# Optimization experiments

Hardware: AMD Instinct MI355X
Metric: run time of the kernel (lower is better)

Reference implementation:

```python
import jax, jax.numpy as jnp
import numpy as np

N_NODES = 100000
N_EDGES = 1600000
N_GRAPHS = 256
EPS = 1e-5  # GraphNorm / BatchNorm eps


def _seg_sum(x, seg, n):
    return jax.ops.segment_sum(x, seg, num_segments=n)


def setup_inputs() -> dict:
    key = jax.random.key(0)
    ks = jax.random.split(key, 24)
    f32 = jnp.float32

    def nrm(k, shape, s=0.05):
        return jax.random.normal(k, shape, f32) * s

    inp = {}
    inp["x"] = jax.random.normal(ks[0], (N_NODES, 64), f32)
    inp["edge_attr"] = jax.random.normal(ks[1], (N_EDGES, 8), f32)
    # edge_mlp: Linear(8,16) -> ReLU -> Linear(16,1); final bias +2 keeps degrees positive
    inp["em_w1"] = nrm(ks[2], (16, 8), 0.1); inp["em_b1"] = jnp.zeros((16,), f32)
    inp["em_w2"] = nrm(ks[3], (1, 16), 0.1); inp["em_b2"] = jnp.full((1,), 2.0, f32)
    # GCNConv weights stored (in, out); PyG GCNConv lin has no bias, separate bias after aggregation
    inp["conv_w0"] = nrm(ks[4], (64, 128)); inp["conv_b0"] = jnp.zeros((128,), f32)
    inp["conv_w1"] = nrm(ks[5], (128, 128)); inp["conv_b1"] = jnp.zeros((128,), f32)
    inp["conv_w2"] = nrm(ks[6], (128, 128)); inp["conv_b2"] = jnp.zeros((128,), f32)
    # GraphNorm params: weight=1, bias=0, mean_scale=1 (PyG init)
    for i in range(3):
        inp[f"gn_w{i}"] = jnp.ones((128,), f32)
        inp[f"gn_b{i}"] = jnp.zeros((128,), f32)
        inp[f"gn_ms{i}"] = jnp.ones((128,), f32)
    # MLP head (weights stored (in,out)); BatchNorm1d eval: running_mean=0, running_var=1
    inp["lin_w0"] = nrm(ks[7], (128, 256)); inp["lin_b0"] = jnp.zeros((256,), f32)
    inp["bn_g0"] = jnp.ones((256,), f32); inp["bn_b0"] = jnp.zeros((256,), f32)
    inp["lin_w1"] = nrm(ks[8], (256, 128)); inp["lin_b1"] = jnp.zeros((128,), f32)
    inp["bn_g1"] = jnp.ones((128,), f32); inp["bn_b1"] = jnp.zeros((128,), f32)
    inp["out_w"] = nrm(ks[9], (128, 1)); inp["out_b"] = jnp.zeros((1,), f32)
    inp["edge_index"] = jax.random.randint(ks[10], (2, N_EDGES), 0, N_NODES)
    inp["batch"] = jnp.sort(jax.random.randint(ks[11], (N_NODES,), 0, N_GRAPHS))
    return inp


def _gcn_conv(h, W, b, src, tgt, ew):
    # PyG GCNConv with edge_weight: add self-loops (weight 1), symmetric normalization
    hw = h @ W  # [N, out]
    deg = _seg_sum(ew, tgt, N_NODES) + 1.0  # in-degree incl. self-loop
    dinv = jnp.where(deg > 0, jax.lax.rsqrt(deg), 0.0)
    norm_e = dinv[src] * ew * dinv[tgt]  # [E]
    agg = _seg_sum(norm_e[:, None] * hw[src], tgt, N_NODES)
    agg = agg + (dinv * dinv)[:, None] * hw  # self-loop contribution
    return agg + b


def _graph_norm(h, batch, w, b, ms, cnt):
    mean = _seg_sum(h, batch, N_GRAPHS) / cnt[:, None]  # [G, C]
    sub = h - ms * mean[batch]
    var = _seg_sum(sub * sub, batch, N_GRAPHS) / cnt[:, None]
    return w * sub / jnp.sqrt(var + EPS)[batch] + b


def reference(x, edge_attr, em_w1, em_b1, em_w2, em_b2,
              conv_w0, conv_b0, conv_w1, conv_b1, conv_w2, conv_b2,
              gn_w0, gn_b0, gn_ms0, gn_w1, gn_b1, gn_ms1, gn_w2, gn_b2, gn_ms2,
              lin_w0, lin_b0, bn_g0, bn_b0, lin_w1, lin_b1, bn_g1, bn_b1,
              out_w, out_b, edge_index, batch):
    src, tgt = edge_index[0], edge_index[1]
    ew = (jax.nn.relu(edge_attr @ em_w1.T + em_b1) @ em_w2.T + em_b2).reshape(-1)  # [E]
    cnt = jnp.maximum(_seg_sum(jnp.ones((N_NODES,), x.dtype), batch, N_GRAPHS), 1.0)

    h = x
    layers = [(conv_w0, conv_b0, gn_w0, gn_b0, gn_ms0),
              (conv_w1, conv_b1, gn_w1, gn_b1, gn_ms1),
              (conv_w2, conv_b2, gn_w2, gn_b2, gn_ms2)]
    for W, b, gw, gb, gms in layers:
        h = _gcn_conv(h, W, b, src, tgt, ew)
        h = _graph_norm(h, batch, gw, gb, gms, cnt)
        h = jax.nn.relu(h)  # dropout is identity in eval mode

    pooled = _seg_sum(h, batch, N_GRAPHS) / cnt[:, None]  # global_mean_pool [G, 128]

    inv = 1.0 / jnp.sqrt(1.0 + EPS)  # BatchNorm1d eval: mean=0, var=1
    h = jax.nn.relu((pooled @ lin_w0 + lin_b0) * inv * bn_g0 + bn_b0)
    h = jax.nn.relu((h @ lin_w1 + lin_b1) * inv * bn_g1 + bn_b1)
    out = h @ out_w + out_b  # [G, 1]
    return (out, h)
```

## Files before the change

### kernel.cpp

```cpp
#include <hip/hip_runtime.h>

#define N_NODES 100000
#define N_EDGES 1600000
#define N_GRAPHS 256
#define EPS 1e-5f

#define NBUCK 1024
#define NUSED 782
#define NBLK 256
#define EPB (N_EDGES / NBLK)

#define WB 128
#define W0B 32
#define SB 2
#define PREP_BLOCKS (WB + W0B + SB + NBLK)

typedef __attribute__((ext_vector_type(8))) short bfrag8;
typedef __attribute__((ext_vector_type(4))) float facc4;

__device__ __forceinline__ void fma4(float4& a, float s, const float4& w) {
  a.x += s * w.x; a.y += s * w.y; a.z += s * w.z; a.w += s * w.w;
}

__device__ __forceinline__ unsigned short f2bf(float f) {
  union { float f; unsigned u; } x;
  x.f = f;
  unsigned r = x.u + 0x7FFF + ((x.u >> 16) & 1);
  return (unsigned short)(r >> 16);
}
__device__ __forceinline__ unsigned packbf(float a, float b) {
  return (unsigned)f2bf(a) | ((unsigned)f2bf(b) << 16);
}
__device__ __forceinline__ float4 bf4(unsigned lo, unsigned hi) {
  union { unsigned u; float f; } a, b, c, d;
  a.u = lo << 16;
  b.u = lo & 0xFFFF0000u;
  c.u = hi << 16;
  d.u = hi & 0xFFFF0000u;
  return make_float4(a.f, b.f, c.f, d.f);
}
__device__ __forceinline__ float bfat(const unsigned* tb, int idx) {
  unsigned u = tb[idx >> 1];
  union { unsigned u; float f; } v;
  v.u = (idx & 1) ? (u & 0xFFFF0000u) : (u << 16);
  return v.f;
}

__global__ __launch_bounds__(256) void k_prep(
    const float* __restrict__ cw1, const float* __restrict__ cw2,
    unsigned short* __restrict__ wt1, unsigned short* __restrict__ wt2,
    const float* __restrict__ cw0, unsigned short* __restrict__ wt0,
    const int* __restrict__ batch, int* __restrict__ start,
    const int* __restrict__ tgt, int* __restrict__ hists) {
  __shared__ int h[NBUCK];
  const int b = blockIdx.x;
  const int t = threadIdx.x;
  if (b < WB) {
    int half = b >> 6;
    int id = (b & 63) * 256 + t;
    const float* w = half ? cw2 : cw1;
    unsigned short* o = half ? wt2 : wt1;
    int n = id >> 7, k = id & 127;
    o[n * 128 + k] = f2bf(w[k * 128 + n]);
  } else if (b < WB + W0B) {
    int id = (b - WB) * 256 + t;
    if (id >= 8192) return;
    int n = id >> 6, k = id & 63;
    wt0[n * 64 + k] = f2bf(cw0[k * 128 + n]);
  } else if (b < WB + W0B + SB) {
    int g = (b - WB - W0B) * 256 + t;
    if (g > N_GRAPHS) return;
    int lo = 0, hi = N_NODES;
    while (lo < hi) {
      int mid = (lo + hi) >> 1;
      if (batch[mid] < g) lo = mid + 1; else hi = mid;
    }
    start[g] = lo;
  } else {
    const int blk = b - WB - W0B - SB;
    for (int i = t; i < NBUCK; i += 256) h[i] = 0;
    __syncthreads();
    const int s = blk * EPB, e = s + EPB;
    for (int j = s + t; j < e; j += 256) atomicAdd(&h[tgt[j] >> 7], 1);
    __syncthreads();
    for (int i = t; i < NBUCK; i += 256) hists[blk * NBUCK + i] = h[i];
  }
}

__global__ __launch_bounds__(1024) void k_bscan(const int* __restrict__ hists,
                                                int* __restrict__ bbase,
                                                int* __restrict__ cursor) {
  __shared__ int s[NBUCK];
  const int b = threadIdx.x;
  int tot = 0;
  for (int k = 0; k < NBLK; ++k) tot += hists[k * NBUCK + b];
  s[b] = tot;
  __syncthreads();
  for (int off = 1; off < NBUCK; off <<= 1) {
    int u = (b >= off) ? s[b - off] : 0;
    __syncthreads();
    s[b] += u;
    __syncthreads();
  }
  int base = s[b] - tot;
  bbase[b] = base;
  if (b == NBUCK - 1) bbase[NBUCK] = N_EDGES;
  int c = base;
  for (int k = 0; k < NBLK; ++k) {
    cursor[k * NBUCK + b] = c;
    c += hists[k * NBUCK + b];
  }
}

__global__ __launch_bounds__(256) void k_scatter(
    const float* __restrict__ ea, const float* __restrict__ w1,
    const float* __restrict__ b1, const float* __restrict__ w2,
    const float* __restrict__ b2, const int* __restrict__ src,
    const int* __restrict__ tgt, const int* __restrict__ cursor,
    uint2* __restrict__ mb) {
  __shared__ float W1[128], B1[16], W2[16];
  __shared__ int cur[NBUCK];
  const int blk = blockIdx.x, t = threadIdx.x;
  if (t < 128) W1[t] = w1[t];
  if (t < 16) { B1[t] = b1[t]; W2[t] = w2[t]; }
  for (int i = t; i < NBUCK; i += 256) cur[i] = cursor[blk * NBUCK + i];
  __syncthreads();
  const int s = blk * EPB, e = s + EPB;
  for (int j = s + t; j < e; j += 256) {
    const float4* ap = (const float4*)(ea + (size_t)j * 8);
    float4 a0 = ap[0], a1 = ap[1];
    float a[8] = {a0.x, a0.y, a0.z, a0.w, a1.x, a1.y, a1.z, a1.w};
    float out = b2[0];
#pragma unroll
    for (int i = 0; i < 16; ++i) {
      float h = B1[i];
#pragma unroll
      for (int jj = 0; jj < 8; ++jj) h += a[jj] * W1[i * 8 + jj];
      out += fmaxf(h, 0.f) * W2[i];
    }
    int d = tgt[j];
    int bin = d >> 7;
    int pos = atomicAdd(&cur[bin], 1);
    union { float f; unsigned u; } w;
    w.f = out;
    mb[pos] = make_uint2(w.u, (unsigned)src[j] | ((unsigned)(d & 127) << 25));
  }
}

__global__ __launch_bounds__(256) void k_csr(const uint2* __restrict__ mb,
                                             const int* __restrict__ bbase,
                                             uint2* __restrict__ meta,
                                             int* __restrict__ rowstart,
                                             float* __restrict__ dinv) {
  __shared__ int hist[128];
  __shared__ float degf[128];
  __shared__ int cur[128];
  const int b = blockIdx.x;
  const int t = threadIdx.x;
  const int s = bbase[b], e = bbase[b + 1];
  if (t < 128) { hist[t] = 0; degf[t] = 0.f; }
  __syncthreads();
  for (int j = s + t; j < e; j += 256) {
    uint2 m = mb[j];
    int bin = m.y >> 25;
    atomicAdd(&hist[bin], 1);
    union { unsigned u; float f; } w;
    w.u = m.x;
    atomicAdd(&degf[bin], w.f);
  }
  __syncthreads();
  int own = (t < 128) ? hist[t] : 0;
  for (int off = 1; off < 128; off <<= 1) {
    int u = (t >= off && t < 128) ? hist[t - off] : 0;
    __syncthreads();
    if (t < 128) hist[t] += u;
    __syncthreads();
  }
  if (t < 128) {
    int excl = hist[t] - own;
    int node = b * 128 + t;
    if (node <= N_NODES) rowstart[node] = s + excl;
    if (node < N_NODES) {
      float d = 1.f + degf[t];
      dinv[node] = d > 0.f ? rsqrtf(d) : 0.f;
    }
    cur[t] = s + excl;
  }
  __syncthreads();
  for (int j = s + t; j < e; j += 256) {
    uint2 m = mb[j];
    int bin = m.y >> 25;
    int pos = atomicAdd(&cur[bin], 1);
    meta[pos] = make_uint2(m.x, m.y & 0x1FFFFFFu);
  }
}

__global__ __launch_bounds__(256) void k_cvt(const float* __restrict__ x,
                                             const float* __restrict__ dinv,
                                             unsigned* __restrict__ xb) {
  int i = blockIdx.x * 256 + threadIdx.x;
  if (i >= N_NODES * 8) return;
  int n = i >> 3;
  float dv = dinv[n];
  const float4* p = (const float4*)(x + (size_t)i * 8);
  float4 a = p[0], b = p[1];
  uint4 o;
  o.x = packbf(dv * a.x, dv * a.y);
  o.y = packbf(dv * a.z, dv * a.w);
  o.z = packbf(dv * b.x, dv * b.y);
  o.w = packbf(dv * b.z, dv * b.w);
  ((uint4*)xb)[i] = o;
}

__global__ __launch_bounds__(256) void k_gather64b(
    const unsigned* __restrict__ xb, const uint2* __restrict__ meta,
    const int* __restrict__ rowstart, const float* __restrict__ dinv,
    unsigned* __restrict__ aggxb) {
  const int t = threadIdx.x;
  const int n = blockIdx.x * 4 + (t >> 6);
  if (n >= N_NODES) return;
  const unsigned lane = t & 63;
  const unsigned q = lane >> 3;
  const unsigned cl = lane & 7;
  const int rs = rowstart[n], re = rowstart[n + 1];
  const uint4* x4 = (const uint4*)xb;
  float4 lo0 = make_float4(0.f, 0.f, 0.f, 0.f), hi0 = lo0;
  float4 lo1 = lo0, hi1 = lo0;
  int j = rs;
  for (; j + 16 <= re; j += 16) {
    uint2 m0 = meta[j + q], m1 = meta[j + 8 + q];
    union { unsigned u; float f; } w0, w1;
    w0.u = m0.x; w1.u = m1.x;
    uint4 v0 = x4[(m0.y << 3) + cl];
    uint4 v1 = x4[(m1.y << 3) + cl];
    fma4(lo0, w0.f, bf4(v0.x, v0.y));
    fma4(hi0, w0.f, bf4(v0.z, v0.w));
    fma4(lo1, w1.f, bf4(v1.x, v1.y));
    fma4(hi1, w1.f, bf4(v1.z, v1.w));
  }
  for (; j + 8 <= re; j += 8) {
    uint2 m0 = meta[j + q];
    union { unsigned u; float f; } w0;
    w0.u = m0.x;
    uint4 v0 = x4[(m0.y << 3) + cl];
    fma4(lo0, w0.f, bf4(v0.x, v0.y));
    fma4(hi0, w0.f, bf4(v0.z, v0.w));
  }
  if (j + (int)q < re) {
    uint2 m0 = meta[j + q];
    union { unsigned u; float f; } w0;
    w0.u = m0.x;
    uint4 v0 = x4[(m0.y << 3) + cl];
    fma4(lo1, w0.f, bf4(v0.x, v0.y));
    fma4(hi1, w0.f, bf4(v0.z, v0.w));
  }
  lo0.x += lo1.x; lo0.y += lo1.y; lo0.z += lo1.z; lo0.w += lo1.w;
  hi0.x += hi1.x; hi0.y += hi1.y; hi0.z += hi1.z; hi0.w += hi1.w;
#pragma unroll
  for (int m = 8; m <= 32; m <<= 1) {
    lo0.x += __shfl_xor(lo0.x, m);
    lo0.y += __shfl_xor(lo0.y, m);
    lo0.z += __shfl_xor(lo0.z, m);
    lo0.w += __shfl_xor(lo0.w, m);
    hi0.x += __shfl_xor(hi0.x, m);
    hi0.y += __shfl_xor(hi0.y, m);
    hi0.z += __shfl_xor(hi0.z, m);
    hi0.w += __shfl_xor(hi0.w, m);
  }
  if (q == 0) {
    float dv = dinv[n];
    uint4 sv = x4[((unsigned)n << 3) + cl];
    float4 slo = bf4(sv.x, sv.y), shi = bf4(sv.z, sv.w);
    uint4 o;
    o.x = packbf(dv * (lo0.x + slo.x), dv * (lo0.y + slo.y));
    o.y = packbf(dv * (lo0.z + slo.z), dv * (lo0.w + slo.w));
    o.z = packbf(dv * (hi0.x + shi.x), dv * (hi0.y + shi.y));
    o.w = packbf(dv * (hi0.z + shi.z), dv * (hi0.w + shi.w));
    ((uint4*)aggxb)[((unsigned)n << 3) + cl] = o;
  }
}

__global__ __launch_bounds__(256) void k_hw_mfma0(
    const unsigned short* __restrict__ aggxb,
    const unsigned short* __restrict__ wt0, const float* __restrict__ bias,
    unsigned short* __restrict__ h1b) {
  __shared__ unsigned short Asb[64][72];
  __shared__ unsigned short Wsb[128][72];
  const int t = threadIdx.x;
  const int base = blockIdx.x * 64;

  for (int i = t; i < 1024; i += 256) {
    int nr = i >> 3, k8 = (i & 7) * 8;
    *(uint4*)&Wsb[nr][k8] = *(const uint4*)&wt0[nr * 64 + k8];
  }
  {
    const int ln = t >> 2;
    const int kp = (t & 3) * 16;
    const int n = base + ln;
    if (n < N_NODES) {
      *(uint4*)&Asb[ln][kp] = *(const uint4*)&aggxb[(size_t)n * 64 + kp];
      *(uint4*)&Asb[ln][kp + 8] = *(const uint4*)&aggxb[(size_t)n * 64 + kp + 8];
    } else {
      uint4 z = make_uint4(0, 0, 0, 0);
      *(uint4*)&Asb[ln][kp] = z;
      *(uint4*)&Asb[ln][kp + 8] = z;
    }
  }
  __syncthreads();

  const int wv = t >> 6;
  const int lr = t & 15;
  const int lk = (t >> 4) & 3;
  const int m0 = wv * 16;

  bfrag8 af[2];
#pragma unroll
  for (int kc = 0; kc < 2; ++kc)
    af[kc] = *(const bfrag8*)&Asb[m0 + lr][kc * 32 + lk * 8];

#pragma unroll
  for (int nt = 0; nt < 8; ++nt) {
    facc4 c = {0.f, 0.f, 0.f, 0.f};
#pragma unroll
    for (int kc = 0; kc < 2; ++kc) {
      bfrag8 bf = *(const bfrag8*)&Wsb[nt * 16 + lr][kc * 32 + lk * 8];
      c = __builtin_amdgcn_mfma_f32_16x16x32_bf16(af[kc], bf, c, 0, 0, 0);
    }
    int col = nt * 16 + lr;
    float bv = bias[col];
#pragma unroll
    for (int r = 0; r < 4; ++r) {
      int n = base + m0 + lk * 4 + r;
      if (n < N_NODES) h1b[(size_t)n * 128 + col] = f2bf(c[r] + bv);
    }
  }
}

__global__ __launch_bounds__(256) void k_hw_mfma(
    const unsigned* __restrict__ hb, const unsigned short* __restrict__ wt,
    const int* __restrict__ batch, const float* __restrict__ An,
    const float* __restrict__ Bn, const float* __restrict__ dinv,
    unsigned short* __restrict__ hwb) {
  __shared__ unsigned short Asb[64][136];
  __shared__ unsigned short Wsb[128][136];
  const int t = threadIdx.x;
  const int base = blockIdx.x * 64;

  for (int i = t; i < 2048; i += 256) {
    int nr = i >> 4, k8 = (i & 15) * 8;
    *(uint4*)&Wsb[nr][k8] = *(const uint4*)&wt[nr * 128 + k8];
  }
  {
    const int ln = t >> 2;
    const int cg = (t & 3) * 32;
    const int n = base + ln;
    if (n < N_NODES) {
      const int g = batch[n];
      const uint4* hp = (const uint4*)(hb + (size_t)n * 64);
      const float* Ap = An + (size_t)g * 128;
      const float* Bp = Bn + (size_t)g * 128;
#pragma unroll
      for (int qq = 0; qq < 4; ++qq) {
        int c = cg + qq * 8;
        uint4 v = hp[(t & 3) * 4 + qq];
        float4 lo = bf4(v.x, v.y);
        float4 hi = bf4(v.z, v.w);
        float4 Alo = *(const float4*)&Ap[c], Blo = *(const float4*)&Bp[c];
        float4 Ahi = *(const float4*)&Ap[c + 4], Bhi = *(const float4*)&Bp[c + 4];
        uint4 o;
        o.x = packbf(fmaxf(Alo.x * lo.x + Blo.x, 0.f),
                     fmaxf(Alo.y * lo.y + Blo.y, 0.f));
        o.y = packbf(fmaxf(Alo.z * lo.z + Blo.z, 0.f),
                     fmaxf(Alo.w * lo.w + Blo.w, 0.f));
        o.z = packbf(fmaxf(Ahi.x * hi.x + Bhi.x, 0.f),
                     fmaxf(Ahi.y * hi.y + Bhi.y, 0.f));
        o.w = packbf(fmaxf(Ahi.z * hi.z + Bhi.z, 0.f),
                     fmaxf(Ahi.w * hi.w + Bhi.w, 0.f));
        *(uint4*)&Asb[ln][c] = o;
      }
    } else {
      uint4 z = make_uint4(0, 0, 0, 0);
#pragma unroll
      for (int qq = 0; qq < 4; ++qq) *(uint4*)&Asb[ln][cg + qq * 8] = z;
    }
  }
  __syncthreads();

  const int wv = t >> 6;
  const int lr = t & 15;
  const int lk = (t >> 4) & 3;
  const int m0 = wv * 16;

  bfrag8 af[4];
#pragma unroll
  for (int kc = 0; kc < 4; ++kc)
    af[kc] = *(const bfrag8*)&Asb[m0 + lr][kc * 32 + lk * 8];

  float dv[4];
#pragma unroll
  for (int r = 0; r < 4; ++r) {
    int n = base + m0 + lk * 4 + r;
    dv[r] = (n < N_NODES) ? dinv[n] : 0.f;
  }

#pragma unroll
  for (int nt = 0; nt < 8; ++nt) {
    facc4 c = {0.f, 0.f, 0.f, 0.f};
#pragma unroll
    for (int kc = 0; kc < 4; ++kc) {
      bfrag8 bf = *(const bfrag8*)&Wsb[nt * 16 + lr][kc * 32 + lk * 8];
      c = __builtin_amdgcn_mfma_f32_16x16x32_bf16(af[kc], bf, c, 0, 0, 0);
    }
    int col = nt * 16 + lr;
#pragma unroll
    for (int r = 0; r < 4; ++r) {
      int n = base + m0 + lk * 4 + r;
      if (n < N_NODES) hwb[(size_t)n * 128 + col] = f2bf(dv[r] * c[r]);
    }
  }
}

__global__ __launch_bounds__(256) void k_gatherb(
    const unsigned* __restrict__ hwb, const uint2* __restrict__ meta,
    const int* __restrict__ rowstart, const float* __restrict__ dinv,
    const float* __restrict__ bias, unsigned* __restrict__ aggb) {
  const int t = threadIdx.x;
  const int n = blockIdx.x * 4 + (t >> 6);
  if (n >= N_NODES) return;
  const unsigned lane = t & 63;
  const unsigned q = lane >> 4;
  const unsigned cl = lane & 15;
  const int rs = rowstart[n], re = rowstart[n + 1];
  const uint4* hb4 = (const uint4*)hwb;
  float4 lo0 = make_float4(0.f, 0.f, 0.f, 0.f), hi0 = lo0;
  float4 lo1 = lo0, hi1 = lo0;
  int j = rs;
  for (; j + 8 <= re; j += 8) {
    uint2 m0 = meta[j + q], m1 = meta[j + 4 + q];
    union { unsigned u; float f; } w0, w1;
    w0.u = m0.x; w1.u = m1.x;
    uint4 v0 = hb4[(m0.y << 4) + cl];
    uint4 v1 = hb4[(m1.y << 4) + cl];
    fma4(lo0, w0.f, bf4(v0.x, v0.y));
    fma4(hi0, w0.f, bf4(v0.z, v0.w));
    fma4(lo1, w1.f, bf4(v1.x, v1.y));
    fma4(hi1, w1.f, bf4(v1.z, v1.w));
  }
  for (; j + 4 <= re; j += 4) {
    uint2 m0 = meta[j + q];
    union { unsigned u; float f; } w0;
    w0.u = m0.x;
    uint4 v0 = hb4[(m0.y << 4) + cl];
    fma4(lo0, w0.f, bf4(v0.x, v0.y));
    fma4(hi0, w0.f, bf4(v0.z, v0.w));
  }
  if (j + (int)q < re) {
    uint2 m0 = meta[j + q];
    union { unsigned u; float f; } w0;
    w0.u = m0.x;
    uint4 v0 = hb4[(m0.y << 4) + cl];
    fma4(lo1, w0.f, bf4(v0.x, v0.y));
    fma4(hi1, w0.f, bf4(v0.z, v0.w));
  }
  lo0.x += lo1.x; lo0.y += lo1.y; lo0.z += lo1.z; lo0.w += lo1.w;
  hi0.x += hi1.x; hi0.y += hi1.y; hi0.z += hi1.z; hi0.w += hi1.w;
#pragma unroll
  for (int m = 16; m <= 32; m <<= 1) {
    lo0.x += __shfl_xor(lo0.x, m);
    lo0.y += __shfl_xor(lo0.y, m);
    lo0.z += __shfl_xor(lo0.z, m);
    lo0.w += __shfl_xor(lo0.w, m);
    hi0.x += __shfl_xor(hi0.x, m);
    hi0.y += __shfl_xor(hi0.y, m);
    hi0.z += __shfl_xor(hi0.z, m);
    hi0.w += __shfl_xor(hi0.w, m);
  }
  if (q == 0) {
    float dv = dinv[n];
    uint4 sv = hb4[((unsigned)n << 4) + cl];
    float4 slo = bf4(sv.x, sv.y), shi = bf4(sv.z, sv.w);
    float4 blo = *(const float4*)&bias[cl * 8];
    float4 bhi = *(const float4*)&bias[cl * 8 + 4];
    uint4 o;
    o.x = packbf(dv * (lo0.x + slo.x) + blo.x, dv * (lo0.y + slo.y) + blo.y);
    o.y = packbf(dv * (lo0.z + slo.z) + blo.z, dv * (lo0.w + slo.w) + blo.w);
    o.z = packbf(dv * (hi0.x + shi.x) + bhi.x, dv * (hi0.y + shi.y) + bhi.y);
    o.w = packbf(dv * (hi0.z + shi.z) + bhi.z, dv * (hi0.w + shi.w) + bhi.w);
    ((uint4*)aggb)[((unsigned)n << 4) + cl] = o;
  }
}

__global__ __launch_bounds__(512) void k_gstats(
    const unsigned* __restrict__ hb, const int* __restrict__ start,
    const float* __restrict__ gw, const float* __restrict__ gb,
    const float* __restrict__ gms, float* __restrict__ An,
    float* __restrict__ Bn) {
  int g = blockIdx.x;
  int s = start[g], e = start[g + 1];
  int t = threadIdx.x, p = t >> 7, c = t & 127;
  float sum = 0.f, sq = 0.f;
  for (int n = s + p; n < e; n += 4) {
    float v = bfat(hb + (size_t)n * 64, c);
    sum += v;
    sq += v * v;
  }
  __shared__ float S[4][128], Q[4][128];
  S[p][c] = sum;
  Q[p][c] = sq;
  __syncthreads();
  if (t < 128) {
    float cnt = (float)max(e - s, 1);
    float mean = (S[0][t] + S[1][t] + S[2][t] + S[3][t]) / cnt;
    float e2 = (Q[0][t] + Q[1][t] + Q[2][t] + Q[3][t]) / cnt;
    float ms = gms[t];
    float var = fmaxf(e2 - ms * (2.f - ms) * mean * mean, 0.f);
    float scale = gw[t] / sqrtf(var + EPS);
    An[(size_t)g * 128 + t] = scale;
    Bn[(size_t)g * 128 + t] = gb[t] - scale * ms * mean;
  }
}

__global__ __launch_bounds__(512) void k_pool(
    const unsigned* __restrict__ hb, const int* __restrict__ start,
    const float* __restrict__ An, const float* __restrict__ Bn,
    float* __restrict__ pooled) {
  int g = blockIdx.x;
  int s = start[g], e = start[g + 1];
  int t = threadIdx.x, p = t >> 7, c = t & 127;
  float A = An[(size_t)g * 128 + c], B = Bn[(size_t)g * 128 + c];
  float sum = 0.f;
  for (int n = s + p; n < e; n += 4)
    sum += fmaxf(A * bfat(hb + (size_t)n * 64, c) + B, 0.f);
  __shared__ float S[4][128];
  S[p][c] = sum;
  __syncthreads();
  if (t < 128) {
    float cnt = (float)max(e - s, 1);
    pooled[g * 128 + t] = (S[0][t] + S[1][t] + S[2][t] + S[3][t]) / cnt;
  }
}

__global__ __launch_bounds__(256) void k_head(
    const float* __restrict__ pooled, const float* __restrict__ w0,
    const float* __restrict__ b0, const float* __restrict__ g0,
    const float* __restrict__ bb0, const float* __restrict__ w1,
    const float* __restrict__ b1, const float* __restrict__ g1,
    const float* __restrict__ bb1, const float* __restrict__ ow,
    const float* __restrict__ ob, float* __restrict__ out) {
  __shared__ float p[128], h1[256], h2[128];
  int g = blockIdx.x, t = threadIdx.x;
  const float inv = 1.0f / sqrtf(1.0f + EPS);
  if (t < 128) p[t] = pooled[g * 128 + t];
  __syncthreads();
  {
    float acc = b0[t];
#pragma unroll 8
    for (int k = 0; k < 128; ++k) acc += p[k] * w0[k * 256 + t];
    h1[t] = fmaxf(acc * inv * g0[t] + bb0[t], 0.f);
  }
  __syncthreads();
  if (t < 128) {
    float acc = b1[t];
#pragma unroll 8
    for (int k = 0; k < 256; ++k) acc += h1[k] * w1[k * 128 + t];
    float v = fmaxf(acc * inv * g1[t] + bb1[t], 0.f);
    h2[t] = v;
    out[N_GRAPHS + g * 128 + t] = v;
  }
  __syncthreads();
  if (t < 64) {
    float v = h2[t] * ow[t] + h2[t + 64] * ow[t + 64];
#pragma unroll
    for (int off = 32; off; off >>= 1) v += __shfl_down(v, off);
    if (t == 0) out[g] = v + ob[0];
  }
}

extern "C" void kernel_launch(void* const* d_in, const int* in_sizes, int n_in,
                              void* d_out, int out_size, void* d_ws,
                              size_t ws_size, hipStream_t stream) {
  const float* x = (const float*)d_in[0];
  const float* edge_attr = (const float*)d_in[1];
  const float* em_w1 = (const float*)d_in[2];
  const float* em_b1 = (const float*)d_in[3];
  const float* em_w2 = (const float*)d_in[4];
  const float* em_b2 = (const float*)d_in[5];
  const float* conv_w[3] = {(const float*)d_in[6], (const float*)d_in[8],
                            (const float*)d_in[10]};
  const float* conv_b[3] = {(const float*)d_in[7], (const float*)d_in[9],
                            (const float*)d_in[11]};
  const float* gn_w[3] = {(const float*)d_in[12], (const float*)d_in[15],
                          (const float*)d_in[18]};
  const float* gn_b[3] = {(const float*)d_in[13], (const float*)d_in[16],
                          (const float*)d_in[19]};
  const float* gn_ms[3] = {(const float*)d_in[14], (const float*)d_in[17],
                           (const float*)d_in[20]};
  const float* lin_w0 = (const float*)d_in[21];
  const float* lin_b0 = (const float*)d_in[22];
  const float* bn_g0 = (const float*)d_in[23];
  const float* bn_b0 = (const float*)d_in[24];
  const float* lin_w1 = (const float*)d_in[25];
  const float* lin_b1 = (const float*)d_in[26];
  const float* bn_g1 = (const float*)d_in[27];
  const float* bn_b1 = (const float*)d_in[28];
  const float* out_w = (const float*)d_in[29];
  const float* out_b = (const float*)d_in[30];
  const int* edge_index = (const int*)d_in[31];
  const int* batch = (const int*)d_in[32];
  const int* src = edge_index;
  const int* tgt = edge_index + N_EDGES;

  char* w = (char*)d_ws;
  size_t off = 0;
  auto carve = [&](size_t bytes) {
    void* p = w + off;
    off = (off + bytes + 511) & ~(size_t)511;
    return p;
  };
  float* dinv = (float*)carve((size_t)N_NODES * 4);
  int* rowstart = (int*)carve((size_t)(N_NODES + 1) * 4);
  int* hists = (int*)carve((size_t)NBLK * NBUCK * 4);
  int* cursor = (int*)carve((size_t)NBLK * NBUCK * 4);
  int* bbase = (int*)carve((size_t)(NBUCK + 1) * 4);
  uint2* mb = (uint2*)carve((size_t)N_EDGES * 8);
  uint2* meta = (uint2*)carve((size_t)N_EDGES * 8);
  int* start = (int*)carve((N_GRAPHS + 1) * 4);
  float* AB = (float*)carve((size_t)6 * N_GRAPHS * 128 * 4);
  unsigned* xb = (unsigned*)carve((size_t)N_NODES * 64 * 2);
  unsigned* aggxb = (unsigned*)carve((size_t)N_NODES * 64 * 2);
  unsigned* h1b = (unsigned*)carve((size_t)N_NODES * 128 * 2);
  unsigned* hwb = (unsigned*)carve((size_t)N_NODES * 128 * 2);
  unsigned* agg1b = (unsigned*)carve((size_t)N_NODES * 128 * 2);
  unsigned* agg2b = (unsigned*)carve((size_t)N_NODES * 128 * 2);
  unsigned short* wt0 = (unsigned short*)carve((size_t)128 * 64 * 2);
  unsigned short* wt1 = (unsigned short*)carve((size_t)128 * 128 * 2);
  unsigned short* wt2 = (unsigned short*)carve((size_t)128 * 128 * 2);
  float* pooled = (float*)carve((size_t)N_GRAPHS * 128 * 4);

  float* A0 = AB, *B0 = AB + N_GRAPHS * 128;
  float* A1 = AB + 2 * N_GRAPHS * 128, *B1 = AB + 3 * N_GRAPHS * 128;
  float* A2 = AB + 4 * N_GRAPHS * 128, *B2 = AB + 5 * N_GRAPHS * 128;

  k_prep<<<PREP_BLOCKS, 256, 0, stream>>>(conv_w[1], conv_w[2], wt1, wt2,
                                          conv_w[0], wt0, batch, start, tgt,
                                          hists);
  k_bscan<<<1, 1024, 0, stream>>>(hists, bbase, cursor);
  k_scatter<<<NBLK, 256, 0, stream>>>(edge_attr, em_w1, em_b1, em_w2, em_b2,
                                      src, tgt, cursor, mb);
  k_csr<<<NUSED, 256, 0, stream>>>(mb, bbase, meta, rowstart, dinv);
  k_cvt<<<(N_NODES * 8 + 255) / 256, 256, 0, stream>>>(x, dinv, xb);

  const int ggrid = (N_NODES + 3) / 4;
  const int hwgrid = (N_NODES + 63) / 64;

  k_gather64b<<<ggrid, 256, 0, stream>>>(xb, meta, rowstart, dinv, aggxb);
  k_hw_mfma0<<<hwgrid, 256, 0, stream>>>((unsigned short*)aggxb, wt0,
                                         conv_b[0], (unsigned short*)h1b);
  k_gstats<<<N_GRAPHS, 512, 0, stream>>>(h1b, start, gn_w[0], gn_b[0],
                                         gn_ms[0], A0, B0);
  k_hw_mfma<<<hwgrid, 256, 0, stream>>>(h1b, wt1, batch, A0, B0, dinv,
                                        (unsigned short*)hwb);
  k_gatherb<<<ggrid, 256, 0, stream>>>(hwb, meta, rowstart, dinv, conv_b[1],
                                       agg1b);
  k_gstats<<<N_GRAPHS, 512, 0, stream>>>(agg1b, start, gn_w[1], gn_b[1],
                                         gn_ms[1], A1, B1);
  k_hw_mfma<<<hwgrid, 256, 0, stream>>>(agg1b, wt2, batch, A1, B1, dinv,
                                        (unsigned short*)hwb);
  k_gatherb<<<ggrid, 256, 0, stream>>>(hwb, meta, rowstart, dinv, conv_b[2],
                                       agg2b);
  k_gstats<<<N_GRAPHS, 512, 0, stream>>>(agg2b, start, gn_w[2], gn_b[2],
                                         gn_ms[2], A2, B2);

  k_pool<<<N_GRAPHS, 512, 0, stream>>>(agg2b, start, A2, B2, pooled);
  k_head<<<N_GRAPHS, 256, 0, stream>>>(pooled, lin_w0, lin_b0, bn_g0, bn_b0,
                                       lin_w1, lin_b1, bn_g1, bn_b1, out_w,
                                       out_b, (float*)d_out);
}
```

Measured before the change: 500.8 us.

## Parallelize bucket scan, fuse bf16 convert into CSR build, merge last stats with pooling

Per-bucket totals are now accumulated with global atomics during the histogram pass. The serial single-block cursor computation is replaced by a parallel per-bucket scan kernel over blocks, with cursors stored transposed. The x-to-bf16 scaling is folded into the CSR kernel using the dinv values already held in shared memory, which removes one launch. The final GraphNorm statistics and mean-pool are merged into one kernel. Together these remove serial loops and launches in exchange for an extra memset, an extra kernel and a second read of the last layer's features.

```diff
diff --git a/kernel.cpp b/kernel.cpp
--- a/kernel.cpp
+++ b/kernel.cpp
@@ -51,7 +51,8 @@
     unsigned short* __restrict__ wt1, unsigned short* __restrict__ wt2,
     const float* __restrict__ cw0, unsigned short* __restrict__ wt0,
     const int* __restrict__ batch, int* __restrict__ start,
-    const int* __restrict__ tgt, int* __restrict__ hists) {
+    const int* __restrict__ tgt, int* __restrict__ hists,
+    int* __restrict__ bcnt) {
   __shared__ int h[NBUCK];
   const int b = blockIdx.x;
   const int t = threadIdx.x;
@@ -83,18 +84,20 @@
     const int s = blk * EPB, e = s + EPB;
     for (int j = s + t; j < e; j += 256) atomicAdd(&h[tgt[j] >> 7], 1);
     __syncthreads();
-    for (int i = t; i < NBUCK; i += 256) hists[blk * NBUCK + i] = h[i];
-  }
-}
-
-__global__ __launch_bounds__(1024) void k_bscan(const int* __restrict__ hists,
-                                                int* __restrict__ bbase,
-                                                int* __restrict__ cursor) {
+    for (int i = t; i < NBUCK; i += 256) {
+      int v = h[i];
+      hists[blk * NBUCK + i] = v;
+      if (v) atomicAdd(&bcnt[i], v);
+    }
+  }
+}
+
+__global__ __launch_bounds__(1024) void k_bscan(const int* __restrict__ bcnt,
+                                                int* __restrict__ bbase) {
   __shared__ int s[NBUCK];
   const int b = threadIdx.x;
-  int tot = 0;
-  for (int k = 0; k < NBLK; ++k) tot += hists[k * NBUCK + b];
-  s[b] = tot;
+  int v = bcnt[b];
+  s[b] = v;
   __syncthreads();
   for (int off = 1; off < NBUCK; off <<= 1) {
     int u = (b >= off) ? s[b - off] : 0;
@@ -102,14 +105,26 @@
     s[b] += u;
     __syncthreads();
   }
-  int base = s[b] - tot;
-  bbase[b] = base;
+  bbase[b] = s[b] - v;
   if (b == NBUCK - 1) bbase[NBUCK] = N_EDGES;
-  int c = base;
-  for (int k = 0; k < NBLK; ++k) {
-    cursor[k * NBUCK + b] = c;
-    c += hists[k * NBUCK + b];
-  }
+}
+
+__global__ __launch_bounds__(NBLK) void k_cursors(const int* __restrict__ hists,
+                                                  const int* __restrict__ bbase,
+                                                  int* __restrict__ cursor) {
+  __shared__ int s[NBLK];
+  const int b = blockIdx.x;
+  const int k = threadIdx.x;
+  int v = hists[k * NBUCK + b];
+  s[k] = v;
+  __syncthreads();
+  for (int off = 1; off < NBLK; off <<= 1) {
+    int u = (k >= off) ? s[k - off] : 0;
+    __syncthreads();
+    s[k] += u;
+    __syncthreads();
+  }
+  cursor[b * NBLK + k] = bbase[b] + s[k] - v;
 }
 
 __global__ __launch_bounds__(256) void k_scatter(
@@ -123,7 +138,7 @@
   const int blk = blockIdx.x, t = threadIdx.x;
   if (t < 128) W1[t] = w1[t];
   if (t < 16) { B1[t] = b1[t]; W2[t] = w2[t]; }
-  for (int i = t; i < NBUCK; i += 256) cur[i] = cursor[blk * NBUCK + i];
+  for (int i = t; i < NUSED; i += 256) cur[i] = cursor[i * NBLK + blk];
   __syncthreads();
   const int s = blk * EPB, e = s + EPB;
   for (int j = s + t; j < e; j += 256) {
@@ -147,14 +162,15 @@
   }
 }
 
-__global__ __launch_bounds__(256) void k_csr(const uint2* __restrict__ mb,
-                                             const int* __restrict__ bbase,
-                                             uint2* __restrict__ meta,
-                                             int* __restrict__ rowstart,
-                                             float* __restrict__ dinv) {
+__global__ __launch_bounds__(256) void k_csr(
+    const uint2* __restrict__ mb, const int* __restrict__ bbase,
+    const float* __restrict__ x, uint2* __restrict__ meta,
+    int* __restrict__ rowstart, float* __restrict__ dinv,
+    unsigned* __restrict__ xb) {
   __shared__ int hist[128];
   __shared__ float degf[128];
   __shared__ int cur[128];
+  __shared__ float dls[128];
   const int b = blockIdx.x;
   const int t = threadIdx.x;
   const int s = bbase[b], e = bbase[b + 1];
@@ -180,10 +196,13 @@
     int excl = hist[t] - own;
     int node = b * 128 + t;
     if (node <= N_NODES) rowstart[node] = s + excl;
+    float dv = 0.f;
     if (node < N_NODES) {
       float d = 1.f + degf[t];
-      dinv[node] = d > 0.f ? rsqrtf(d) : 0.f;
-    }
+      dv = d > 0.f ? rsqrtf(d) : 0.f;
+      dinv[node] = dv;
+    }
+    dls[t] = dv;
     cur[t] = s + excl;
   }
   __syncthreads();
@@ -193,23 +212,25 @@
     int pos = atomicAdd(&cur[bin], 1);
     meta[pos] = make_uint2(m.x, m.y & 0x1FFFFFFu);
   }
-}
-
-__global__ __launch_bounds__(256) void k_cvt(const float* __restrict__ x,
-                                             const float* __restrict__ dinv,
-                                             unsigned* __restrict__ xb) {
-  int i = blockIdx.x * 256 + threadIdx.x;
-  if (i >= N_NODES * 8) return;
-  int n = i >> 3;
-  float dv = dinv[n];
-  const float4* p = (const float4*)(x + (size_t)i * 8);
-  float4 a = p[0], b = p[1];
-  uint4 o;
-  o.x = packbf(dv * a.x, dv * a.y);
-  o.y = packbf(dv * a.z, dv * a.w);
-  o.z = packbf(dv * b.x, dv * b.y);
-  o.w = packbf(dv * b.z, dv * b.w);
-  ((uint4*)xb)[i] = o;
+  {
+    const int ln = t >> 1, half = t & 1;
+    const int node = b * 128 + ln;
+    if (node < N_NODES) {
+      float dv = dls[ln];
+      const float* px = x + (size_t)node * 64 + half * 32;
+#pragma unroll
+      for (int c8 = 0; c8 < 4; ++c8) {
+        float4 a = *(const float4*)(px + c8 * 8);
+        float4 bb = *(const float4*)(px + c8 * 8 + 4);
+        uint4 o;
+        o.x = packbf(dv * a.x, dv * a.y);
+        o.y = packbf(dv * a.z, dv * a.w);
+        o.z = packbf(dv * bb.x, dv * bb.y);
+        o.w = packbf(dv * bb.z, dv * bb.w);
+        *(uint4*)&xb[(size_t)node * 32 + half * 16 + c8 * 4] = o;
+      }
+    }
+  }
 }
 
 __global__ __launch_bounds__(256) void k_gather64b(
@@ -520,19 +541,40 @@
   }
 }
 
-__global__ __launch_bounds__(512) void k_pool(
+__global__ __launch_bounds__(512) void k_gstats_pool(
     const unsigned* __restrict__ hb, const int* __restrict__ start,
-    const float* __restrict__ An, const float* __restrict__ Bn,
-    float* __restrict__ pooled) {
+    const float* __restrict__ gw, const float* __restrict__ gb,
+    const float* __restrict__ gms, float* __restrict__ pooled) {
   int g = blockIdx.x;
   int s = start[g], e = start[g + 1];
   int t = threadIdx.x, p = t >> 7, c = t & 127;
-  float A = An[(size_t)g * 128 + c], B = Bn[(size_t)g * 128 + c];
-  float sum = 0.f;
+  float sum = 0.f, sq = 0.f;
+  for (int n = s + p; n < e; n += 4) {
+    float v = bfat(hb + (size_t)n * 64, c);
+    sum += v;
+    sq += v * v;
+  }
+  __shared__ float S[4][128], Q[4][128], Af[128], Bf[128];
+  S[p][c] = sum;
+  Q[p][c] = sq;
+  __syncthreads();
+  if (t < 128) {
+    float cnt = (float)max(e - s, 1);
+    float mean = (S[0][t] + S[1][t] + S[2][t] + S[3][t]) / cnt;
+    float e2 = (Q[0][t] + Q[1][t] + Q[2][t] + Q[3][t]) / cnt;
+    float ms = gms[t];
+    float var = fmaxf(e2 - ms * (2.f - ms) * mean * mean, 0.f);
+    float scale = gw[t] / sqrtf(var + EPS);
+    Af[t] = scale;
+    Bf[t] = gb[t] - scale * ms * mean;
+  }
+  __syncthreads();
+  float A = Af[c], B = Bf[c];
+  float psum = 0.f;
   for (int n = s + p; n < e; n += 4)
-    sum += fmaxf(A * bfat(hb + (size_t)n * 64, c) + B, 0.f);
-  __shared__ float S[4][128];
-  S[p][c] = sum;
+    psum += fmaxf(A * bfat(hb + (size_t)n * 64, c) + B, 0.f);
+  __syncthreads();
+  S[p][c] = psum;
   __syncthreads();
   if (t < 128) {
     float cnt = (float)max(e - s, 1);
@@ -620,12 +662,13 @@
   float* dinv = (float*)carve((size_t)N_NODES * 4);
   int* rowstart = (int*)carve((size_t)(N_NODES + 1) * 4);
   int* hists = (int*)carve((size_t)NBLK * NBUCK * 4);
-  int* cursor = (int*)carve((size_t)NBLK * NBUCK * 4);
+  int* cursor = (int*)carve((size_t)NBUCK * NBLK * 4);
+  int* bcnt = (int*)carve((size_t)NBUCK * 4);
   int* bbase = (int*)carve((size_t)(NBUCK + 1) * 4);
   uint2* mb = (uint2*)carve((size_t)N_EDGES * 8);
   uint2* meta = (uint2*)carve((size_t)N_EDGES * 8);
   int* start = (int*)carve((N_GRAPHS + 1) * 4);
-  float* AB = (float*)carve((size_t)6 * N_GRAPHS * 128 * 4);
+  float* AB = (float*)carve((size_t)4 * N_GRAPHS * 128 * 4);
   unsigned* xb = (unsigned*)carve((size_t)N_NODES * 64 * 2);
   unsigned* aggxb = (unsigned*)carve((size_t)N_NODES * 64 * 2);
   unsigned* h1b = (unsigned*)carve((size_t)N_NODES * 128 * 2);
@@ -639,16 +682,17 @@
 
   float* A0 = AB, *B0 = AB + N_GRAPHS * 128;
   float* A1 = AB + 2 * N_GRAPHS * 128, *B1 = AB + 3 * N_GRAPHS * 128;
-  float* A2 = AB + 4 * N_GRAPHS * 128, *B2 = AB + 5 * N_GRAPHS * 128;
+
+  hipMemsetAsync(bcnt, 0, (size_t)NBUCK * 4, stream);
 
   k_prep<<<PREP_BLOCKS, 256, 0, stream>>>(conv_w[1], conv_w[2], wt1, wt2,
                                           conv_w[0], wt0, batch, start, tgt,
-                                          hists);
-  k_bscan<<<1, 1024, 0, stream>>>(hists, bbase, cursor);
+                                          hists, bcnt);
+  k_bscan<<<1, 1024, 0, stream>>>(bcnt, bbase);
+  k_cursors<<<NUSED, NBLK, 0, stream>>>(hists, bbase, cursor);
   k_scatter<<<NBLK, 256, 0, stream>>>(edge_attr, em_w1, em_b1, em_w2, em_b2,
                                       src, tgt, cursor, mb);
-  k_csr<<<NUSED, 256, 0, stream>>>(mb, bbase, meta, rowstart, dinv);
-  k_cvt<<<(N_NODES * 8 + 255) / 256, 256, 0, stream>>>(x, dinv, xb);
+  k_csr<<<NUSED, 256, 0, stream>>>(mb, bbase, x, meta, rowstart, dinv, xb);
 
   const int ggrid = (N_NODES + 3) / 4;
   const int hwgrid = (N_NODES + 63) / 64;
@@ -668,10 +712,9 @@
                                         (unsigned short*)hwb);
   k_gatherb<<<ggrid, 256, 0, stream>>>(hwb, meta, rowstart, dinv, conv_b[2],
                                        agg2b);
-  k_gstats<<<N_GRAPHS, 512, 0, stream>>>(agg2b, start, gn_w[2], gn_b[2],
-                                         gn_ms[2], A2, B2);
-
-  k_pool<<<N_GRAPHS, 512, 0, stream>>>(agg2b, start, A2, B2, pooled);
+  k_gstats_pool<<<N_GRAPHS, 512, 0, stream>>>(agg2b, start, gn_w[2], gn_b[2],
+                                              gn_ms[2], pooled);
+
   k_head<<<N_GRAPHS, 256, 0, stream>>>(pooled, lin_w0, lin_b0, bn_g0, bn_b0,
                                        lin_w1, lin_b1, bn_g1, bn_b1, out_w,
                                        out_b, (float*)d_out);
```

Measured after the change: 489.4 us. -2.3%, faster.
